# Kernel tuning notes

Measured on AMD Instinct MI355X. Metric: run time of the kernel, lower is better.

Reference implementation:

```python
import jax, jax.numpy as jnp
import numpy as np

B, QL, KL = 2, 1024, 4096
H = 1024          # hidden_size
NH = 16           # num_heads
HD = H // NH      # head_dim = 64


def setup_inputs() -> dict:
    key = jax.random.key(0)
    k1, k2, k3, k4, k5 = jax.random.split(key, 5)
    s = 1.0 / np.sqrt(H)
    return {
        "query": jax.random.normal(k1, (B, QL, H), dtype=jnp.float32),
        "key_value": jax.random.normal(k2, (B, KL, H), dtype=jnp.float32),
        "w_q": jax.random.uniform(k3, (H, H), dtype=jnp.float32, minval=-s, maxval=s),
        "w_kv": jax.random.uniform(k4, (H, 2 * H), dtype=jnp.float32, minval=-s, maxval=s),
        "w_out": jax.random.uniform(k5, (H, H), dtype=jnp.float32, minval=-s, maxval=s),
    }


def reference(query, key_value, w_q, w_kv, w_out):
    # projections
    q = (query @ w_q).reshape(B, QL, NH, HD).transpose(0, 2, 1, 3)      # [B,NH,QL,HD]
    kv = (key_value @ w_kv).reshape(B, KL, 2, NH, HD)
    k = kv[:, :, 0].transpose(0, 2, 1, 3)                               # [B,NH,KL,HD]
    v = kv[:, :, 1].transpose(0, 2, 1, 3)                               # [B,NH,KL,HD]
    # scaled dot-product attention (explicit, matching source)
    scale = 1.0 / np.sqrt(HD).astype(np.float32)
    attn = jnp.einsum("bhqd,bhkd->bhqk", q, k) * scale                  # [B,NH,QL,KL]
    attn = jax.nn.softmax(attn, axis=-1)
    out = jnp.einsum("bhqk,bhkd->bhqd", attn, v)                        # [B,NH,QL,HD]
    out = out.transpose(0, 2, 1, 3).reshape(B, QL, H)
    return out @ w_out
```

## Files before the change

### kernel.cpp

```cpp
#include <hip/hip_runtime.h>

#define Bb   2
#define QL   1024
#define KL   4096
#define Hh   1024
#define NH   16
#define HD   64

#define KSPLIT 2
#define CHUNK  (KL / KSPLIT)
#define NTT    (CHUNK / 64)

typedef unsigned short u16;
typedef __attribute__((ext_vector_type(8))) short bf16x8;
typedef __attribute__((ext_vector_type(8))) unsigned short usv8;
typedef __attribute__((ext_vector_type(4))) float f32x4;

#define QSCALE 0.1803368801111204f
#define RTHR   11.0f

__device__ __forceinline__ u16 f2bf(float f) {
    union { float f; unsigned int u; } v; v.f = f;
    unsigned int r = (v.u + 0x7FFFu + ((v.u >> 16) & 1u)) >> 16;
    return (u16)r;
}

__device__ __forceinline__ unsigned int cvt_pk_bf16(float lo, float hi) {
    unsigned int r;
    asm("v_cvt_pk_bf16_f32 %0, %1, %2" : "=v"(r) : "v"(lo), "v"(hi));
    return r;
}

__device__ __forceinline__ float max3f(float a, float b, float c) {
    float r;
    asm("v_max3_f32 %0, %1, %2, %3" : "=v"(r) : "v"(a), "v"(b), "v"(c));
    return r;
}

__device__ __forceinline__ void gload16(const void* g, void* l) {
    __builtin_amdgcn_global_load_lds(
        (const __attribute__((address_space(1))) void*)g,
        (__attribute__((address_space(3))) void*)l, 16, 0, 0);
}

__device__ __forceinline__ uint4 pack8(const float4& f0, const float4& f1) {
    uint4 o;
    o.x = cvt_pk_bf16(f0.x, f0.y);
    o.y = cvt_pk_bf16(f0.z, f0.w);
    o.z = cvt_pk_bf16(f1.x, f1.y);
    o.w = cvt_pk_bf16(f1.z, f1.w);
    return o;
}

__global__ __launch_bounds__(256) void cast_all(const float* __restrict__ q,
                                                const float* __restrict__ kv,
                                                u16* __restrict__ qb,
                                                u16* __restrict__ kvb) {
    int bid = blockIdx.x;
    const float* in; u16* out;
    if (bid < 1024) { in = q;  out = qb;  }
    else            { in = kv; out = kvb; bid -= 1024; }
    const size_t i = ((size_t)bid * 256 + threadIdx.x) * 8;
    float4 f0 = *reinterpret_cast<const float4*>(in + i);
    float4 f1 = *reinterpret_cast<const float4*>(in + i + 4);
    *reinterpret_cast<uint4*>(out + i) = pack8(f0, f1);
}

__global__ __launch_bounds__(256) void wtrans_all(const float* __restrict__ wq,
                                                  const float* __restrict__ wkv,
                                                  const float* __restrict__ wout,
                                                  u16* __restrict__ wqT,
                                                  u16* __restrict__ wkvT,
                                                  u16* __restrict__ woutT) {
    __shared__ float T[64][65];
    int bid = blockIdx.x;
    const float* in; u16* out; int C;
    if (bid < 256)      { in = wq;   out = wqT;   C = 1024; }
    else if (bid < 768) { in = wkv;  out = wkvT;  C = 2048; bid -= 256; }
    else                { in = wout; out = woutT; C = 1024; bid -= 768; }
    const int nc = C >> 6;
    const int c0 = (bid % nc) * 64;
    const int r0 = (bid / nc) * 64;
    const int t  = threadIdx.x;
    const int tx = t & 15, ty = t >> 4;
#pragma unroll
    for (int p = 0; p < 4; ++p) {
        const int r = ty + p * 16;
        float4 v = *reinterpret_cast<const float4*>(in + (size_t)(r0 + r) * C + c0 + tx * 4);
        T[r][tx * 4 + 0] = v.x; T[r][tx * 4 + 1] = v.y;
        T[r][tx * 4 + 2] = v.z; T[r][tx * 4 + 3] = v.w;
    }
    __syncthreads();
#pragma unroll
    for (int p = 0; p < 4; ++p) {
        const int c = ty + p * 16;
        const int n = c0 + c;
        ushort4 o;
        o.x = f2bf(T[tx * 4 + 0][c]); o.y = f2bf(T[tx * 4 + 1][c]);
        o.z = f2bf(T[tx * 4 + 2][c]); o.w = f2bf(T[tx * 4 + 3][c]);
        const int kb   = r0 + tx * 4;
        const int kout = (kb & ~63) | ((((kb >> 3) & 7) ^ (n & 7)) << 3) | (kb & 7);
        *reinterpret_cast<ushort4*>(out + (size_t)n * 1024 + kout) = o;
    }
}

__global__ __launch_bounds__(256) void qkvgemm(const u16* __restrict__ Aq,
                                               const u16* __restrict__ Akv,
                                               const u16* __restrict__ wqT,
                                               const u16* __restrict__ wkvT,
                                               u16* __restrict__ Qb,
                                               u16* __restrict__ KT,
                                               u16* __restrict__ VT) {
    __shared__ u16 As[128 * 64];
    __shared__ u16 Bs[128 * 64];
    const int tid = threadIdx.x, lane = tid & 63, w = tid >> 6;
    const int wr = w >> 1, wc = w & 1;
    const int x7 = lane & 7;
    const int lrow = lane >> 3, lcol = (lane & 7) * 8;
    const int swcol = lcol ^ ((lrow & 7) << 3);

    if (blockIdx.x < 1024) {
        const int id = blockIdx.x;
        const int sw = (id & 7) * 128 + (id >> 3);
        const int bx = sw % 16, by = sw / 16;
        const int row0 = by * 128, col0 = bx * 128;
        const int MROW = wr * 64;

        f32x4 acc[4][4];
#pragma unroll
        for (int m = 0; m < 4; ++m)
#pragma unroll
            for (int n = 0; n < 4; ++n) acc[m][n] = (f32x4){0.f, 0.f, 0.f, 0.f};

        auto stage = [&](int k0) {
            __syncthreads();
#pragma unroll
            for (int p = 0; p < 4; ++p) {
                const int base = w * 512 + p * 2048;
                const int row  = (base >> 6) + lrow;
                gload16(Akv + (size_t)(row0 + row) * 1024 + k0 + swcol, &As[base]);
                gload16(wkvT + (size_t)(col0 + row) * 1024 + k0 + lcol, &Bs[base]);
            }
            __syncthreads();
        };

        if (col0 < 1024) {
            for (int k0 = 0; k0 < 1024; k0 += 64) {
                stage(k0);
#pragma unroll
                for (int kk = 0; kk < 2; ++kk) {
                    bf16x8 af[4], bfr[4];
                    const int G = ((kk * 4 + (lane >> 4)) ^ x7) * 8;
#pragma unroll
                    for (int m = 0; m < 4; ++m)
                        af[m] = *reinterpret_cast<const bf16x8*>(
                            &As[(MROW + m * 16 + (lane & 15)) * 64 + G]);
#pragma unroll
                    for (int n = 0; n < 4; ++n)
                        bfr[n] = *reinterpret_cast<const bf16x8*>(
                            &Bs[(wc * 64 + n * 16 + (lane & 15)) * 64 + G]);
#pragma unroll
                    for (int m = 0; m < 4; ++m)
#pragma unroll
                        for (int n = 0; n < 4; ++n)
                            acc[m][n] = __builtin_amdgcn_mfma_f32_16x16x32_bf16(
                                bfr[n], af[m], acc[m][n], 0, 0, 0);
                }
            }
#pragma unroll
            for (int m = 0; m < 4; ++m) {
                const int gr  = row0 + MROW + m * 16 + (lane & 15);
                const int b   = gr >> 12;
                const int k   = gr & 4095;
                const int kt_i = k >> 6, k_in = k & 63;
#pragma unroll
                for (int n = 0; n < 4; ++n) {
                    const int gc0 = col0 + wc * 64 + n * 16 + (lane >> 4) * 4;
                    const int h   = gc0 >> 6, d0 = gc0 & 63;
                    u16* blob = KT + (((size_t)((b << 4) + h) * 64 + kt_i) << 9) * 8;
                    const int og = k_in * 8 + ((d0 >> 3) ^ (k_in & 7));
                    ushort4 pk;
                    pk.x = f2bf(acc[m][n][0]); pk.y = f2bf(acc[m][n][1]);
                    pk.z = f2bf(acc[m][n][2]); pk.w = f2bf(acc[m][n][3]);
                    *reinterpret_cast<ushort4*>(&blob[og * 8 + (d0 & 7)]) = pk;
                }
            }
        } else {
            for (int k0 = 0; k0 < 1024; k0 += 64) {
                stage(k0);
#pragma unroll
                for (int kk = 0; kk < 2; ++kk) {
                    bf16x8 af[4], bfr[4];
                    const int G = ((kk * 4 + (lane >> 4)) ^ x7) * 8;
#pragma unroll
                    for (int m = 0; m < 4; ++m)
                        af[m] = *reinterpret_cast<const bf16x8*>(
                            &As[(MROW + m * 16 + (lane & 15)) * 64 + G]);
#pragma unroll
                    for (int n = 0; n < 4; ++n)
                        bfr[n] = *reinterpret_cast<const bf16x8*>(
                            &Bs[(wc * 64 + n * 16 + (lane & 15)) * 64 + G]);
#pragma unroll
                    for (int m = 0; m < 4; ++m)
#pragma unroll
                        for (int n = 0; n < 4; ++n)
                            acc[m][n] = __builtin_amdgcn_mfma_f32_16x16x32_bf16(
                                af[m], bfr[n], acc[m][n], 0, 0, 0);
                }
            }
#pragma unroll
            for (int m = 0; m < 4; ++m) {
                const int gr0 = row0 + MROW + m * 16 + (lane >> 4) * 4;
                const int b   = gr0 >> 12;
                const int k   = gr0 & 4095;
                const int kt_i = k >> 6, k_in = k & 63;
#pragma unroll
                for (int n = 0; n < 4; ++n) {
                    const int gc = col0 + wc * 64 + n * 16 + (lane & 15);
                    const int h  = (gc & 1023) >> 6, d = gc & 63;
                    u16* blob = VT + (((size_t)((b << 4) + h) * 64 + kt_i) << 9) * 8;
                    const int og = d * 8 + ((k_in >> 3) ^ (d & 7));
                    ushort4 pk;
                    pk.x = f2bf(acc[m][n][0]); pk.y = f2bf(acc[m][n][1]);
                    pk.z = f2bf(acc[m][n][2]); pk.w = f2bf(acc[m][n][3]);
                    *reinterpret_cast<ushort4*>(&blob[og * 8 + (k_in & 7)]) = pk;
                }
            }
        }
    } else {
        const int id = blockIdx.x - 1024;
        const int sw = (id & 7) * 32 + (id >> 3);
        const int bx = sw % 8, by = sw / 8;
        const int row0 = by * 64, col0 = bx * 128;
        const int MROW = wr * 32;

        f32x4 acc[2][4];
#pragma unroll
        for (int m = 0; m < 2; ++m)
#pragma unroll
            for (int n = 0; n < 4; ++n) acc[m][n] = (f32x4){0.f, 0.f, 0.f, 0.f};

        for (int k0 = 0; k0 < 1024; k0 += 64) {
            __syncthreads();
#pragma unroll
            for (int p = 0; p < 2; ++p) {
                const int base = w * 512 + p * 2048;
                const int row  = (base >> 6) + lrow;
                gload16(Aq + (size_t)(row0 + row) * 1024 + k0 + swcol, &As[base]);
            }
#pragma unroll
            for (int p = 0; p < 4; ++p) {
                const int base = w * 512 + p * 2048;
                const int row  = (base >> 6) + lrow;
                gload16(wqT + (size_t)(col0 + row) * 1024 + k0 + lcol, &Bs[base]);
            }
            __syncthreads();
#pragma unroll
            for (int kk = 0; kk < 2; ++kk) {
                bf16x8 af[2], bfr[4];
                const int G = ((kk * 4 + (lane >> 4)) ^ x7) * 8;
#pragma unroll
                for (int m = 0; m < 2; ++m)
                    af[m] = *reinterpret_cast<const bf16x8*>(
                        &As[(MROW + m * 16 + (lane & 15)) * 64 + G]);
#pragma unroll
                for (int n = 0; n < 4; ++n)
                    bfr[n] = *reinterpret_cast<const bf16x8*>(
                        &Bs[(wc * 64 + n * 16 + (lane & 15)) * 64 + G]);
#pragma unroll
                for (int m = 0; m < 2; ++m)
#pragma unroll
                    for (int n = 0; n < 4; ++n)
                        acc[m][n] = __builtin_amdgcn_mfma_f32_16x16x32_bf16(
                            af[m], bfr[n], acc[m][n], 0, 0, 0);
            }
        }
#pragma unroll
        for (int m = 0; m < 2; ++m)
#pragma unroll
            for (int n = 0; n < 4; ++n) {
                const int gc = col0 + wc * 64 + n * 16 + (lane & 15);
#pragma unroll
                for (int r = 0; r < 4; ++r) {
                    const int gr = row0 + MROW + m * 16 + (lane >> 4) * 4 + r;
                    Qb[(size_t)gr * 1024 + gc] = f2bf(acc[m][n][r] * QSCALE);
                }
            }
    }
}

__global__ __launch_bounds__(256, 2) void attn_mfma(const u16* __restrict__ Qb,
                                                    const u16* __restrict__ KT,
                                                    const u16* __restrict__ VT2,
                                                    float* __restrict__ Op,
                                                    float* __restrict__ m_ws,
                                                    float* __restrict__ l_ws) {
    __shared__ u16 Ks[2][4096];
    __shared__ u16 Vs[2][4096];
    __shared__ u16 Ps[4][2][1024];

    const int bid0 = blockIdx.x;
    const int bid  = (bid0 & 7) * 64 + (bid0 >> 3);
    const int qb   = bid & 7;
    const int h    = (bid >> 3) & 15;
    const int b    = (bid >> 7) & 1;
    const int c    = bid >> 8;
    const int tid  = threadIdx.x;
    const int lane = tid & 63;
    const int w    = tid >> 6;
    const int q_l  = lane & 15;
    const int g    = lane >> 4;
    const int qs7  = q_l & 7;
    const int q0   = qb * 128;
    const int bh   = b * NH + h;

    bf16x8 qa[2][2];
#pragma unroll
    for (int qh = 0; qh < 2; ++qh) {
        const u16* qsrc = Qb + (size_t)(b * QL + q0 + w * 32 + qh * 16 + q_l) * Hh
                          + h * HD + g * 8;
        qa[qh][0] = *reinterpret_cast<const bf16x8*>(qsrc);
        qa[qh][1] = *reinterpret_cast<const bf16x8*>(qsrc + 32);
    }
    asm volatile("s_waitcnt vmcnt(0)" ::: "memory");

    bf16x8 ones;
#pragma unroll
    for (int e = 0; e < 8; ++e) ones[e] = (short)0x3F80;

    float m_i[2] = {-1e30f, -1e30f};
    f32x4 acc_l[2] = {(f32x4){0.f, 0.f, 0.f, 0.f}, (f32x4){0.f, 0.f, 0.f, 0.f}};
    f32x4 acc_o[2][4];
#pragma unroll
    for (int qh = 0; qh < 2; ++qh)
#pragma unroll
        for (int n = 0; n < 4; ++n) acc_o[qh][n] = (f32x4){0.f, 0.f, 0.f, 0.f};

    const int koffA = (g ^ qs7) * 8;
    const int koffB = ((g + 4) ^ qs7) * 8;
    const int rowq  = q_l * 64;
    const u16* KsA[2] = { &Ks[0][rowq + koffA], &Ks[1][rowq + koffA] };
    const u16* KsB[2] = { &Ks[0][rowq + koffB], &Ks[1][rowq + koffB] };
    const u16* VsA[2] = { &Vs[0][rowq + koffA], &Vs[1][rowq + koffA] };
    const u16* VsB[2] = { &Vs[0][rowq + koffB], &Vs[1][rowq + koffB] };
    const u16* PsRA = &Ps[w][0][rowq + koffA];
    const u16* PsRB = &Ps[w][0][rowq + koffB];
    u16* PsW[4];
#pragma unroll
    for (int n = 0; n < 4; ++n)
        PsW[n] = &Ps[w][0][rowq + (((2 * n + (g >> 1)) ^ qs7) << 3) + (g & 1) * 4];

    const size_t tb0 = ((size_t)bh * 64 + c * NTT) * 4096;
    const u16* kpt = KT  + tb0 + (size_t)(w * 64 + lane) * 8 + 1024;
    const u16* vpt = VT2 + tb0 + (size_t)(w * 64 + lane) * 8 + 1024;
    u16* kdst[2] = { &Ks[0][w * 512], &Ks[1][w * 512] };
    u16* vdst[2] = { &Vs[0][w * 512], &Vs[1][w * 512] };

    gload16(kpt - 1024, kdst[0]);
    gload16(kpt + 1024, kdst[0] + 2048);
    gload16(vpt - 1024, vdst[0]);
    gload16(vpt + 1024, vdst[0] + 2048);

    auto tile = [&](int CUR, int t) {
        __builtin_amdgcn_s_barrier();
        if (t + 1 < NTT) {
            kpt += 4096; vpt += 4096;
            gload16(kpt - 1024, kdst[CUR ^ 1]);
            gload16(kpt + 1024, kdst[CUR ^ 1] + 2048);
            gload16(vpt - 1024, vdst[CUR ^ 1]);
            gload16(vpt + 1024, vdst[CUR ^ 1] + 2048);
            asm volatile("s_waitcnt vmcnt(4)" ::: "memory");
        } else {
            asm volatile("s_waitcnt vmcnt(0)" ::: "memory");
        }
        __builtin_amdgcn_sched_barrier(0);
        __builtin_amdgcn_s_barrier();

        f32x4 s[2][4];
        __builtin_amdgcn_s_setprio(1);
#pragma unroll
        for (int n = 0; n < 4; ++n) {
            bf16x8 a0 = *reinterpret_cast<const bf16x8*>(KsA[CUR] + n * 1024);
            bf16x8 a1 = *reinterpret_cast<const bf16x8*>(KsB[CUR] + n * 1024);
#pragma unroll
            for (int qh = 0; qh < 2; ++qh) {
                f32x4 z = (f32x4){0.f, 0.f, 0.f, 0.f};
                z = __builtin_amdgcn_mfma_f32_16x16x32_bf16(a0, qa[qh][0], z, 0, 0, 0);
                z = __builtin_amdgcn_mfma_f32_16x16x32_bf16(a1, qa[qh][1], z, 0, 0, 0);
                s[qh][n] = z;
            }
        }
        __builtin_amdgcn_s_setprio(0);

        float mloc[2];
#pragma unroll
        for (int qh = 0; qh < 2; ++qh) {
            float c1 = max3f(s[qh][0][0], s[qh][0][1], s[qh][0][2]);
            c1 = max3f(c1, s[qh][0][3], s[qh][1][0]);
            c1 = max3f(c1, s[qh][1][1], s[qh][1][2]);
            c1 = fmaxf(c1, s[qh][1][3]);
            float c2 = max3f(s[qh][2][0], s[qh][2][1], s[qh][2][2]);
            c2 = max3f(c2, s[qh][2][3], s[qh][3][0]);
            c2 = max3f(c2, s[qh][3][1], s[qh][3][2]);
            c2 = fmaxf(c2, s[qh][3][3]);
            float m = fmaxf(c1, c2);
            m = fmaxf(m, __shfl_xor(m, 16));
            m = fmaxf(m, __shfl_xor(m, 32));
            mloc[qh] = m;
        }
        if (__any((mloc[0] > m_i[0] + RTHR) || (mloc[1] > m_i[1] + RTHR))) {
#pragma unroll
            for (int qh = 0; qh < 2; ++qh) {
                const float mnew = fmaxf(m_i[qh], mloc[qh]);
                const float al   = exp2f(m_i[qh] - mnew);
                m_i[qh] = mnew;
                acc_l[qh][0] *= al; acc_l[qh][1] *= al;
                acc_l[qh][2] *= al; acc_l[qh][3] *= al;
#pragma unroll
                for (int n = 0; n < 4; ++n) {
                    f32x4 tt = acc_o[qh][n];
                    tt[0] *= al; tt[1] *= al; tt[2] *= al; tt[3] *= al;
                    acc_o[qh][n] = tt;
                }
            }
        }
#pragma unroll
        for (int qh = 0; qh < 2; ++qh) {
#pragma unroll
            for (int n = 0; n < 4; ++n)
#pragma unroll
                for (int r = 0; r < 4; ++r) s[qh][n][r] = exp2f(s[qh][n][r] - m_i[qh]);
#pragma unroll
            for (int n = 0; n < 4; ++n) {
                uint2 pk2;
                pk2.x = cvt_pk_bf16(s[qh][n][0], s[qh][n][1]);
                pk2.y = cvt_pk_bf16(s[qh][n][2], s[qh][n][3]);
                *reinterpret_cast<uint2*>(PsW[n] + qh * 1024) = pk2;
            }
        }
        asm volatile("s_waitcnt lgkmcnt(0)" ::: "memory");
        __builtin_amdgcn_sched_barrier(0);

        __builtin_amdgcn_s_setprio(1);
#pragma unroll
        for (int kf = 0; kf < 2; ++kf) {
            const u16* pr = (kf == 0) ? PsRA : PsRB;
            bf16x8 pf0 = *reinterpret_cast<const bf16x8*>(pr);
            bf16x8 pf1 = *reinterpret_cast<const bf16x8*>(pr + 1024);
            acc_l[0] = __builtin_amdgcn_mfma_f32_16x16x32_bf16(ones, pf0, acc_l[0], 0, 0, 0);
            acc_l[1] = __builtin_amdgcn_mfma_f32_16x16x32_bf16(ones, pf1, acc_l[1], 0, 0, 0);
#pragma unroll
            for (int n = 0; n < 4; ++n) {
                const u16* vb = (kf == 0) ? VsA[CUR] : VsB[CUR];
                bf16x8 vf = *reinterpret_cast<const bf16x8*>(vb + n * 1024);
                acc_o[0][n] = __builtin_amdgcn_mfma_f32_16x16x32_bf16(vf, pf0, acc_o[0][n], 0, 0, 0);
                acc_o[1][n] = __builtin_amdgcn_mfma_f32_16x16x32_bf16(vf, pf1, acc_o[1][n], 0, 0, 0);
            }
        }
        __builtin_amdgcn_s_setprio(0);
    };

    for (int t = 0; t < NTT; t += 2) {
        tile(0, t);
        tile(1, t + 1);
    }

#pragma unroll
    for (int qh = 0; qh < 2; ++qh) {
        float* opc = Op + (size_t)c * ((size_t)Bb * QL * Hh)
                     + (size_t)(b * QL + q0 + w * 32 + qh * 16 + q_l) * Hh + h * HD;
#pragma unroll
        for (int n = 0; n < 4; ++n) {
            float4 v = make_float4(acc_o[qh][n][0], acc_o[qh][n][1],
                                   acc_o[qh][n][2], acc_o[qh][n][3]);
            *reinterpret_cast<float4*>(opc + n * 16 + g * 4) = v;
        }
        if (g == 0) {
            const int idx = ((c * Bb + b) * NH + h) * QL + q0 + w * 32 + qh * 16 + q_l;
            m_ws[idx] = m_i[qh];
            l_ws[idx] = acc_l[qh][0];
        }
    }
}

__global__ __launch_bounds__(256) void ogemm(const float* __restrict__ Op,
                                             const float* __restrict__ m_ws,
                                             const float* __restrict__ l_ws,
                                             const u16* __restrict__ Bt,
                                             float* __restrict__ C) {
    __shared__ u16 As[64 * 64];
    __shared__ u16 Bs[128 * 64];
    const int nwg = gridDim.x * gridDim.y;
    const int id  = blockIdx.y * gridDim.x + blockIdx.x;
    const int sw  = (id & 7) * (nwg >> 3) + (id >> 3);
    const int bx  = sw % gridDim.x, by = sw / gridDim.x;
    const int tid = threadIdx.x, lane = tid & 63, w = tid >> 6;
    const int wr = w >> 1, wc = w & 1;
    const int row0 = by * 64, col0 = bx * 128;
    const int MROW = wr * 32;
    const int x7   = lane & 7;

    f32x4 acc[2][4];
#pragma unroll
    for (int m = 0; m < 2; ++m)
#pragma unroll
        for (int n = 0; n < 4; ++n) acc[m][n] = (f32x4){0.f, 0.f, 0.f, 0.f};

    const int lrow = lane >> 3, lcol = (lane & 7) * 8;
    const int arow = tid >> 3, acol8 = (tid & 7) * 8;
    const int aphys = acol8 ^ ((arow & 7) << 3);

    for (int k0 = 0; k0 < 1024; k0 += 64) {
        __syncthreads();
        const int h_ = k0 >> 6;
#pragma unroll
        for (int p = 0; p < 2; ++p) {
            const int r    = p * 32 + arow;
            const int grow = row0 + r;
            const int b_   = grow >> 10, q_ = grow & 1023;
            const int idx  = (((b_ << 4) + h_) << 10) + q_;
            const float m0 = m_ws[idx], m1 = m_ws[idx + 32768];
            const float l0 = l_ws[idx], l1 = l_ws[idx + 32768];
            const float ms = fmaxf(m0, m1);
            float a0 = exp2f(m0 - ms), a1 = exp2f(m1 - ms);
            const float inv = 1.f / (l0 * a0 + l1 * a1);
            a0 *= inv; a1 *= inv;
            const float* o0 = Op + (size_t)grow * 1024 + k0 + acol8;
            const float* o1 = o0 + (size_t)Bb * QL * Hh;
            float4 x0 = *reinterpret_cast<const float4*>(o0);
            float4 x1 = *reinterpret_cast<const float4*>(o0 + 4);
            float4 y0 = *reinterpret_cast<const float4*>(o1);
            float4 y1 = *reinterpret_cast<const float4*>(o1 + 4);
            float4 f0 = make_float4(x0.x * a0 + y0.x * a1, x0.y * a0 + y0.y * a1,
                                    x0.z * a0 + y0.z * a1, x0.w * a0 + y0.w * a1);
            float4 f1 = make_float4(x1.x * a0 + y1.x * a1, x1.y * a0 + y1.y * a1,
                                    x1.z * a0 + y1.z * a1, x1.w * a0 + y1.w * a1);
            *reinterpret_cast<uint4*>(&As[r * 64 + aphys]) = pack8(f0, f1);
        }
#pragma unroll
        for (int p = 0; p < 4; ++p) {
            const int base = w * 512 + p * 2048;
            const int row  = (base >> 6) + lrow;
            gload16(Bt + (size_t)(col0 + row) * 1024 + k0 + lcol, &Bs[base]);
        }
        __syncthreads();
#pragma unroll
        for (int kk = 0; kk < 2; ++kk) {
            bf16x8 af[2], bfr[4];
            const int G = ((kk * 4 + (lane >> 4)) ^ x7) * 8;
#pragma unroll
            for (int m = 0; m < 2; ++m)
                af[m] = *reinterpret_cast<const bf16x8*>(
                    &As[(MROW + m * 16 + (lane & 15)) * 64 + G]);
#pragma unroll
            for (int n = 0; n < 4; ++n)
                bfr[n] = *reinterpret_cast<const bf16x8*>(
                    &Bs[(wc * 64 + n * 16 + (lane & 15)) * 64 + G]);
#pragma unroll
            for (int m = 0; m < 2; ++m)
#pragma unroll
                for (int n = 0; n < 4; ++n)
                    acc[m][n] = __builtin_amdgcn_mfma_f32_16x16x32_bf16(
                        af[m], bfr[n], acc[m][n], 0, 0, 0);
        }
    }
#pragma unroll
    for (int m = 0; m < 2; ++m)
#pragma unroll
        for (int n = 0; n < 4; ++n) {
            const int gc = col0 + wc * 64 + n * 16 + (lane & 15);
#pragma unroll
            for (int r = 0; r < 4; ++r) {
                const int gr = row0 + MROW + m * 16 + (lane >> 4) * 4 + r;
                C[(size_t)gr * 1024 + gc] = acc[m][n][r];
            }
        }
}

extern "C" void kernel_launch(void* const* d_in, const int* in_sizes, int n_in,
                              void* d_out, int out_size, void* d_ws, size_t ws_size,
                              hipStream_t stream) {
    const float* query     = (const float*)d_in[0];
    const float* key_value = (const float*)d_in[1];
    const float* w_q       = (const float*)d_in[2];
    const float* w_kv      = (const float*)d_in[3];
    const float* w_out     = (const float*)d_in[4];
    float* out = (float*)d_out;

    char* ws = (char*)d_ws;
    const size_t MB = 1024 * 1024;
    u16*   KT    = (u16*)(ws);
    u16*   VT    = (u16*)(ws + 16 * MB);
    u16*   kvbf  = (u16*)(ws + 32 * MB);
    float* Opart = (float*)(ws + 32 * MB);
    u16*   Qb    = (u16*)(ws + 48 * MB);
    u16*   wkvT  = (u16*)(ws + 52 * MB);
    u16*   wqT   = (u16*)(ws + 56 * MB);
    u16*   woutT = (u16*)(ws + 58 * MB);
    float* m_wsp = (float*)(ws + 60 * MB);
    float* l_wsp = (float*)(ws + 60 * MB + 256 * 1024);
    u16*   qbf   = (u16*)(ws + 64 * MB);

    dim3 blk(256);

    wtrans_all<<<1024, blk, 0, stream>>>(w_q, w_kv, w_out, wqT, wkvT, woutT);
    cast_all<<<5120, blk, 0, stream>>>(query, key_value, qbf, kvbf);

    qkvgemm<<<1280, blk, 0, stream>>>(qbf, kvbf, wqT, wkvT, Qb, KT, VT);

    attn_mfma<<<dim3(KSPLIT * 256), blk, 0, stream>>>(
        Qb, KT, VT, Opart, m_wsp, l_wsp);

    ogemm<<<dim3(8, 32), blk, 0, stream>>>(Opart, m_wsp, l_wsp, woutT, out);
}
```

Baseline: 174.5 us.

## Use 32x32x16 MFMA in attention with in-register P via permlane swap

The attention kernel moves from 16x16x32 MFMA tiles to 32x32x16 MFMA, where each wave computes a 32-query by 32-key score block per instruction. Softmax probabilities are repacked in registers with v_permlane32_swap instead of being staged through LDS, and the row sum is computed with VALU adds instead of a ones-MFMA. This drops the P shared-memory buffer, its writes, reads and the lgkmcnt wait, at the cost of more VALU work per lane and a larger accumulator register footprint. Separately, the weight-transpose and activation-cast kernels are merged into one launch to remove a kernel boundary.

```diff
diff --git a/kernel.cpp b/kernel.cpp
--- a/kernel.cpp
+++ b/kernel.cpp
@@ -13,8 +13,8 @@
 
 typedef unsigned short u16;
 typedef __attribute__((ext_vector_type(8))) short bf16x8;
-typedef __attribute__((ext_vector_type(8))) unsigned short usv8;
 typedef __attribute__((ext_vector_type(4))) float f32x4;
+typedef __attribute__((ext_vector_type(16))) float f32x16;
 
 #define QSCALE 0.1803368801111204f
 #define RTHR   11.0f
@@ -35,6 +35,10 @@
     float r;
     asm("v_max3_f32 %0, %1, %2, %3" : "=v"(r) : "v"(a), "v"(b), "v"(c));
     return r;
+}
+
+__device__ __forceinline__ void plane32swap(unsigned int& a, unsigned int& b) {
+    asm volatile("v_permlane32_swap_b32 %0, %1" : "+v"(a), "+v"(b));
 }
 
 __device__ __forceinline__ void gload16(const void* g, void* l) {
@@ -52,28 +56,29 @@
     return o;
 }
 
-__global__ __launch_bounds__(256) void cast_all(const float* __restrict__ q,
-                                                const float* __restrict__ kv,
+__global__ __launch_bounds__(256) void prep_all(const float* __restrict__ wq,
+                                                const float* __restrict__ wkv,
+                                                const float* __restrict__ wout,
+                                                const float* __restrict__ qact,
+                                                const float* __restrict__ kvact,
+                                                u16* __restrict__ wqT,
+                                                u16* __restrict__ wkvT,
+                                                u16* __restrict__ woutT,
                                                 u16* __restrict__ qb,
                                                 u16* __restrict__ kvb) {
-    int bid = blockIdx.x;
-    const float* in; u16* out;
-    if (bid < 1024) { in = q;  out = qb;  }
-    else            { in = kv; out = kvb; bid -= 1024; }
-    const size_t i = ((size_t)bid * 256 + threadIdx.x) * 8;
-    float4 f0 = *reinterpret_cast<const float4*>(in + i);
-    float4 f1 = *reinterpret_cast<const float4*>(in + i + 4);
-    *reinterpret_cast<uint4*>(out + i) = pack8(f0, f1);
-}
-
-__global__ __launch_bounds__(256) void wtrans_all(const float* __restrict__ wq,
-                                                  const float* __restrict__ wkv,
-                                                  const float* __restrict__ wout,
-                                                  u16* __restrict__ wqT,
-                                                  u16* __restrict__ wkvT,
-                                                  u16* __restrict__ woutT) {
     __shared__ float T[64][65];
     int bid = blockIdx.x;
+    if (bid >= 1024) {
+        bid -= 1024;
+        const float* in; u16* out;
+        if (bid < 1024) { in = qact;  out = qb;  }
+        else            { in = kvact; out = kvb; bid -= 1024; }
+        const size_t i = ((size_t)bid * 256 + threadIdx.x) * 8;
+        float4 f0 = *reinterpret_cast<const float4*>(in + i);
+        float4 f1 = *reinterpret_cast<const float4*>(in + i + 4);
+        *reinterpret_cast<uint4*>(out + i) = pack8(f0, f1);
+        return;
+    }
     const float* in; u16* out; int C;
     if (bid < 256)      { in = wq;   out = wqT;   C = 1024; }
     else if (bid < 768) { in = wkv;  out = wkvT;  C = 2048; bid -= 256; }
@@ -297,7 +302,6 @@
                                                     float* __restrict__ l_ws) {
     __shared__ u16 Ks[2][4096];
     __shared__ u16 Vs[2][4096];
-    __shared__ u16 Ps[4][2][1024];
 
     const int bid0 = blockIdx.x;
     const int bid  = (bid0 & 7) * 64 + (bid0 >> 3);
@@ -308,47 +312,34 @@
     const int tid  = threadIdx.x;
     const int lane = tid & 63;
     const int w    = tid >> 6;
-    const int q_l  = lane & 15;
-    const int g    = lane >> 4;
-    const int qs7  = q_l & 7;
+    const int q    = lane & 31;
+    const int hl   = lane >> 5;
+    const int l7   = lane & 7;
     const int q0   = qb * 128;
     const int bh   = b * NH + h;
 
-    bf16x8 qa[2][2];
-#pragma unroll
-    for (int qh = 0; qh < 2; ++qh) {
-        const u16* qsrc = Qb + (size_t)(b * QL + q0 + w * 32 + qh * 16 + q_l) * Hh
-                          + h * HD + g * 8;
-        qa[qh][0] = *reinterpret_cast<const bf16x8*>(qsrc);
-        qa[qh][1] = *reinterpret_cast<const bf16x8*>(qsrc + 32);
+    bf16x8 qa[4];
+    {
+        const u16* qsrc = Qb + (size_t)(b * QL + q0 + w * 32 + q) * Hh
+                          + h * HD + hl * 8;
+#pragma unroll
+        for (int dc = 0; dc < 4; ++dc)
+            qa[dc] = *reinterpret_cast<const bf16x8*>(qsrc + dc * 16);
     }
     asm volatile("s_waitcnt vmcnt(0)" ::: "memory");
 
-    bf16x8 ones;
-#pragma unroll
-    for (int e = 0; e < 8; ++e) ones[e] = (short)0x3F80;
-
-    float m_i[2] = {-1e30f, -1e30f};
-    f32x4 acc_l[2] = {(f32x4){0.f, 0.f, 0.f, 0.f}, (f32x4){0.f, 0.f, 0.f, 0.f}};
-    f32x4 acc_o[2][4];
-#pragma unroll
-    for (int qh = 0; qh < 2; ++qh)
-#pragma unroll
-        for (int n = 0; n < 4; ++n) acc_o[qh][n] = (f32x4){0.f, 0.f, 0.f, 0.f};
-
-    const int koffA = (g ^ qs7) * 8;
-    const int koffB = ((g + 4) ^ qs7) * 8;
-    const int rowq  = q_l * 64;
-    const u16* KsA[2] = { &Ks[0][rowq + koffA], &Ks[1][rowq + koffA] };
-    const u16* KsB[2] = { &Ks[0][rowq + koffB], &Ks[1][rowq + koffB] };
-    const u16* VsA[2] = { &Vs[0][rowq + koffA], &Vs[1][rowq + koffA] };
-    const u16* VsB[2] = { &Vs[0][rowq + koffB], &Vs[1][rowq + koffB] };
-    const u16* PsRA = &Ps[w][0][rowq + koffA];
-    const u16* PsRB = &Ps[w][0][rowq + koffB];
-    u16* PsW[4];
-#pragma unroll
-    for (int n = 0; n < 4; ++n)
-        PsW[n] = &Ps[w][0][rowq + (((2 * n + (g >> 1)) ^ qs7) << 3) + (g & 1) * 4];
+    float m_i = -1e30f, l_i = 0.f;
+    f32x16 accO[2];
+#pragma unroll
+    for (int d2 = 0; d2 < 2; ++d2)
+#pragma unroll
+        for (int r = 0; r < 16; ++r) accO[d2][r] = 0.f;
+
+    const u16* Kb0 = &Ks[0][q * 64];
+    const u16* Vb0 = &Vs[0][q * 64];
+    int off[4];
+#pragma unroll
+    for (int j = 0; j < 4; ++j) off[j] = (((j * 2 + hl) ^ l7) << 3);
 
     const size_t tb0 = ((size_t)bh * 64 + c * NTT) * 4096;
     const u16* kpt = KT  + tb0 + (size_t)(w * 64 + lane) * 8 + 1024;
@@ -376,86 +367,82 @@
         __builtin_amdgcn_sched_barrier(0);
         __builtin_amdgcn_s_barrier();
 
-        f32x4 s[2][4];
+        f32x16 sc[2];
         __builtin_amdgcn_s_setprio(1);
 #pragma unroll
-        for (int n = 0; n < 4; ++n) {
-            bf16x8 a0 = *reinterpret_cast<const bf16x8*>(KsA[CUR] + n * 1024);
-            bf16x8 a1 = *reinterpret_cast<const bf16x8*>(KsB[CUR] + n * 1024);
-#pragma unroll
-            for (int qh = 0; qh < 2; ++qh) {
-                f32x4 z = (f32x4){0.f, 0.f, 0.f, 0.f};
-                z = __builtin_amdgcn_mfma_f32_16x16x32_bf16(a0, qa[qh][0], z, 0, 0, 0);
-                z = __builtin_amdgcn_mfma_f32_16x16x32_bf16(a1, qa[qh][1], z, 0, 0, 0);
-                s[qh][n] = z;
-            }
+        for (int kc = 0; kc < 2; ++kc) {
+            f32x16 z;
+#pragma unroll
+            for (int r = 0; r < 16; ++r) z[r] = 0.f;
+#pragma unroll
+            for (int dc = 0; dc < 4; ++dc) {
+                bf16x8 kf = *reinterpret_cast<const bf16x8*>(
+                    Kb0 + CUR * 4096 + kc * 2048 + off[dc]);
+                z = __builtin_amdgcn_mfma_f32_32x32x16_bf16(kf, qa[dc], z, 0, 0, 0);
+            }
+            sc[kc] = z;
         }
         __builtin_amdgcn_s_setprio(0);
 
-        float mloc[2];
-#pragma unroll
-        for (int qh = 0; qh < 2; ++qh) {
-            float c1 = max3f(s[qh][0][0], s[qh][0][1], s[qh][0][2]);
-            c1 = max3f(c1, s[qh][0][3], s[qh][1][0]);
-            c1 = max3f(c1, s[qh][1][1], s[qh][1][2]);
-            c1 = fmaxf(c1, s[qh][1][3]);
-            float c2 = max3f(s[qh][2][0], s[qh][2][1], s[qh][2][2]);
-            c2 = max3f(c2, s[qh][2][3], s[qh][3][0]);
-            c2 = max3f(c2, s[qh][3][1], s[qh][3][2]);
-            c2 = fmaxf(c2, s[qh][3][3]);
-            float m = fmaxf(c1, c2);
-            m = fmaxf(m, __shfl_xor(m, 16));
-            m = fmaxf(m, __shfl_xor(m, 32));
-            mloc[qh] = m;
-        }
-        if (__any((mloc[0] > m_i[0] + RTHR) || (mloc[1] > m_i[1] + RTHR))) {
-#pragma unroll
-            for (int qh = 0; qh < 2; ++qh) {
-                const float mnew = fmaxf(m_i[qh], mloc[qh]);
-                const float al   = exp2f(m_i[qh] - mnew);
-                m_i[qh] = mnew;
-                acc_l[qh][0] *= al; acc_l[qh][1] *= al;
-                acc_l[qh][2] *= al; acc_l[qh][3] *= al;
-#pragma unroll
-                for (int n = 0; n < 4; ++n) {
-                    f32x4 tt = acc_o[qh][n];
-                    tt[0] *= al; tt[1] *= al; tt[2] *= al; tt[3] *= al;
-                    acc_o[qh][n] = tt;
-                }
-            }
-        }
-#pragma unroll
-        for (int qh = 0; qh < 2; ++qh) {
-#pragma unroll
-            for (int n = 0; n < 4; ++n)
-#pragma unroll
-                for (int r = 0; r < 4; ++r) s[qh][n][r] = exp2f(s[qh][n][r] - m_i[qh]);
-#pragma unroll
-            for (int n = 0; n < 4; ++n) {
-                uint2 pk2;
-                pk2.x = cvt_pk_bf16(s[qh][n][0], s[qh][n][1]);
-                pk2.y = cvt_pk_bf16(s[qh][n][2], s[qh][n][3]);
-                *reinterpret_cast<uint2*>(PsW[n] + qh * 1024) = pk2;
-            }
-        }
-        asm volatile("s_waitcnt lgkmcnt(0)" ::: "memory");
-        __builtin_amdgcn_sched_barrier(0);
+        float mx = max3f(sc[0][0], sc[0][1], sc[0][2]);
+#pragma unroll
+        for (int i = 3; i + 1 < 32; i += 2)
+            mx = max3f(mx, sc[i >> 4][i & 15], sc[(i + 1) >> 4][(i + 1) & 15]);
+        mx = fmaxf(mx, sc[1][15]);
+        mx = fmaxf(mx, __shfl_xor(mx, 32));
+
+        if (__any(mx > m_i + RTHR)) {
+            const float mnew = fmaxf(m_i, mx);
+            const float al   = exp2f(m_i - mnew);
+            m_i = mnew;
+            l_i *= al;
+#pragma unroll
+            for (int d2 = 0; d2 < 2; ++d2)
+#pragma unroll
+                for (int r = 0; r < 16; ++r) accO[d2][r] *= al;
+        }
+#pragma unroll
+        for (int kc = 0; kc < 2; ++kc)
+#pragma unroll
+            for (int r = 0; r < 16; ++r) sc[kc][r] = exp2f(sc[kc][r] - m_i);
+
+        {
+            float p0 = sc[0][0], p1 = sc[0][1], p2 = sc[0][2], p3 = sc[0][3];
+#pragma unroll
+            for (int i = 4; i < 16; i += 4) {
+                p0 += sc[0][i];     p1 += sc[0][i + 1];
+                p2 += sc[0][i + 2]; p3 += sc[0][i + 3];
+            }
+#pragma unroll
+            for (int i = 0; i < 16; i += 4) {
+                p0 += sc[1][i];     p1 += sc[1][i + 1];
+                p2 += sc[1][i + 2]; p3 += sc[1][i + 3];
+            }
+            float sum = (p0 + p1) + (p2 + p3);
+            sum += __shfl_xor(sum, 32);
+            l_i += sum;
+        }
 
         __builtin_amdgcn_s_setprio(1);
 #pragma unroll
-        for (int kf = 0; kf < 2; ++kf) {
-            const u16* pr = (kf == 0) ? PsRA : PsRB;
-            bf16x8 pf0 = *reinterpret_cast<const bf16x8*>(pr);
-            bf16x8 pf1 = *reinterpret_cast<const bf16x8*>(pr + 1024);
-            acc_l[0] = __builtin_amdgcn_mfma_f32_16x16x32_bf16(ones, pf0, acc_l[0], 0, 0, 0);
-            acc_l[1] = __builtin_amdgcn_mfma_f32_16x16x32_bf16(ones, pf1, acc_l[1], 0, 0, 0);
-#pragma unroll
-            for (int n = 0; n < 4; ++n) {
-                const u16* vb = (kf == 0) ? VsA[CUR] : VsB[CUR];
-                bf16x8 vf = *reinterpret_cast<const bf16x8*>(vb + n * 1024);
-                acc_o[0][n] = __builtin_amdgcn_mfma_f32_16x16x32_bf16(vf, pf0, acc_o[0][n], 0, 0, 0);
-                acc_o[1][n] = __builtin_amdgcn_mfma_f32_16x16x32_bf16(vf, pf1, acc_o[1][n], 0, 0, 0);
-            }
+        for (int kk = 0; kk < 4; ++kk) {
+            const int kc  = kk >> 1;
+            const int rb  = (kk & 1) * 8;
+            unsigned int X0 = cvt_pk_bf16(sc[kc][rb + 0], sc[kc][rb + 1]);
+            unsigned int X1 = cvt_pk_bf16(sc[kc][rb + 2], sc[kc][rb + 3]);
+            unsigned int Y0 = cvt_pk_bf16(sc[kc][rb + 4], sc[kc][rb + 5]);
+            unsigned int Y1 = cvt_pk_bf16(sc[kc][rb + 6], sc[kc][rb + 7]);
+            plane32swap(X0, Y0);
+            plane32swap(X1, Y1);
+            uint4 wv = make_uint4(X0, X1, Y0, Y1);
+            bf16x8 pf;
+            __builtin_memcpy(&pf, &wv, 16);
+            bf16x8 vf0 = *reinterpret_cast<const bf16x8*>(
+                Vb0 + CUR * 4096 + off[kk]);
+            bf16x8 vf1 = *reinterpret_cast<const bf16x8*>(
+                Vb0 + CUR * 4096 + 2048 + off[kk]);
+            accO[0] = __builtin_amdgcn_mfma_f32_32x32x16_bf16(vf0, pf, accO[0], 0, 0, 0);
+            accO[1] = __builtin_amdgcn_mfma_f32_32x32x16_bf16(vf1, pf, accO[1], 0, 0, 0);
         }
         __builtin_amdgcn_s_setprio(0);
     };
@@ -465,21 +452,21 @@
         tile(1, t + 1);
     }
 
-#pragma unroll
-    for (int qh = 0; qh < 2; ++qh) {
-        float* opc = Op + (size_t)c * ((size_t)Bb * QL * Hh)
-                     + (size_t)(b * QL + q0 + w * 32 + qh * 16 + q_l) * Hh + h * HD;
-#pragma unroll
-        for (int n = 0; n < 4; ++n) {
-            float4 v = make_float4(acc_o[qh][n][0], acc_o[qh][n][1],
-                                   acc_o[qh][n][2], acc_o[qh][n][3]);
-            *reinterpret_cast<float4*>(opc + n * 16 + g * 4) = v;
-        }
-        if (g == 0) {
-            const int idx = ((c * Bb + b) * NH + h) * QL + q0 + w * 32 + qh * 16 + q_l;
-            m_ws[idx] = m_i[qh];
-            l_ws[idx] = acc_l[qh][0];
-        }
+    float* opc = Op + (size_t)c * ((size_t)Bb * QL * Hh)
+                 + (size_t)(b * QL + q0 + w * 32 + q) * Hh + h * HD;
+#pragma unroll
+    for (int d2 = 0; d2 < 2; ++d2) {
+#pragma unroll
+        for (int b2 = 0; b2 < 4; ++b2) {
+            float4 v = make_float4(accO[d2][4 * b2 + 0], accO[d2][4 * b2 + 1],
+                                   accO[d2][4 * b2 + 2], accO[d2][4 * b2 + 3]);
+            *reinterpret_cast<float4*>(opc + d2 * 32 + b2 * 8 + hl * 4) = v;
+        }
+    }
+    if (hl == 0) {
+        const int idx = ((c * Bb + b) * NH + h) * QL + q0 + w * 32 + q;
+        m_ws[idx] = m_i;
+        l_ws[idx] = l_i;
     }
 }
 
@@ -603,8 +590,8 @@
 
     dim3 blk(256);
 
-    wtrans_all<<<1024, blk, 0, stream>>>(w_q, w_kv, w_out, wqT, wkvT, woutT);
-    cast_all<<<5120, blk, 0, stream>>>(query, key_value, qbf, kvbf);
+    prep_all<<<6144, blk, 0, stream>>>(w_q, w_kv, w_out, query, key_value,
+                                       wqT, wkvT, woutT, qbf, kvbf);
 
     qkvgemm<<<1280, blk, 0, stream>>>(qbf, kvbf, wqT, wkvT, Qb, KT, VT);
 
```

Measured after the change: 166.9 us. -4.3%, faster.
